# Optimization experiments

Hardware: AMD Instinct MI355X
Metric: run time of the kernel (lower is better)

Reference implementation:

```python
import jax, jax.numpy as jnp
import numpy as np


def setup_inputs() -> dict:
    key = jax.random.key(0)
    k1, k2, k3 = jax.random.split(key, 3)
    B, T, D, U = 64, 1024, 256, 256
    inputs = jax.random.normal(k1, (B, T, D), dtype=jnp.float32)
    W_xh = jax.random.normal(k2, (D, U), dtype=jnp.float32) * (1.0 / np.sqrt(D))
    W_hh = jax.random.normal(k3, (U, U), dtype=jnp.float32) * (1.0 / np.sqrt(U))
    b_h = jnp.zeros((U,), dtype=jnp.float32)
    return {"inputs": inputs, "W_xh": W_xh, "W_hh": W_hh, "b_h": b_h}


def reference(inputs, W_xh, W_hh, b_h):
    # inputs: [B, T, D]. Precompute input projection (same math as per-step matmul),
    # then scan the sequential recurrence: h_t = tanh(xW_t + h_{t-1} @ W_hh + b).
    B = inputs.shape[0]
    U = W_hh.shape[0]
    xW = jnp.einsum('btd,du->btu', inputs, W_xh) + b_h  # [B, T, U]
    h0 = jnp.zeros((B, U), dtype=inputs.dtype)

    def step(h, xw_t):
        h_new = jnp.tanh(xw_t + h @ W_hh)
        return h_new, h_new

    _, hs = jax.lax.scan(step, h0, jnp.swapaxes(xW, 0, 1))  # hs: [T, B, U]
    return jnp.swapaxes(hs, 0, 1)  # [B, T, U] (return_sequences=True)
```

## Files before the change

kernel.cpp:

```cpp
#include <hip/hip_runtime.h>
#include <math.h>

#define B_ 64
#define T_ 1024
#define D_ 256
#define U_ 256

typedef __fp16   hf2_t __attribute__((ext_vector_type(2)));
typedef _Float16 f16x8 __attribute__((ext_vector_type(8)));
typedef float    f32x4 __attribute__((ext_vector_type(4)));

__device__ __forceinline__ float fast_tanh2(float x) {
    float e = __expf(2.0f * x);
    return 1.0f - 2.0f * __builtin_amdgcn_rcpf(e + 1.0f);
}

#define CH_  16
#define NCH_ (T_ / CH_)
#define NT2_ 512

__global__ __launch_bounds__(NT2_) __attribute__((amdgpu_waves_per_eu(2, 2)))
void rnn_fused(const float* __restrict__ inputs,
               const float* __restrict__ W_xh,
               const float* __restrict__ W_hh,
               const float* __restrict__ b_h,
               float* __restrict__ out) {
    const int b    = (int)blockIdx.x;
    const int tid  = (int)threadIdx.x;
    const int w    = tid >> 6;
    const int lane = tid & 63;
    const int g    = lane >> 4;
    const int c    = lane & 15;
    const int n0   = w * 32;

    __shared__ float xwb[2][CH_][U_];
    __shared__ __align__(16) _Float16 hl[2][U_];
    __shared__ __align__(16) _Float16 Ax[CH_ * D_];

    f16x8 whh[8][2], wxh[8][2];
    #pragma unroll
    for (int kt = 0; kt < 8; ++kt) {
        #pragma unroll
        for (int nt = 0; nt < 2; ++nt) {
            f16x8 vh, vx;
            #pragma unroll
            for (int j = 0; j < 8; ++j) {
                const int row = kt * 32 + g * 8 + j;
                const int col = n0 + nt * 16 + c;
                vh[j] = (_Float16)W_hh[(size_t)row * U_ + col];
                vx[j] = (_Float16)W_xh[(size_t)row * U_ + col];
            }
            whh[kt][nt] = vh;
            wxh[kt][nt] = vx;
        }
    }
    const float bb0 = b_h[n0 + c];
    const float bb1 = b_h[n0 + 16 + c];

    if (tid < 128) ((float*)&hl[0][0])[tid] = 0.f;

    const float* ibase = inputs + (size_t)b * T_ * D_;
    float* gbase = out + (size_t)b * T_ * U_;

    const int srow = tid >> 5;
    const int sk8  = (tid & 31) * 8;
    char* const sdst = (char*)Ax + srow * 512 + ((sk8 * 2) ^ ((srow & 7) << 4));
    const int vbaseA = c * 512 + ((g * 16) ^ ((c & 7) << 4));

    const f32x4 zero4 = {0.f, 0.f, 0.f, 0.f};

#define PACK8(DST, F0, F1)                                                    \
    {                                                                         \
        union { hf2_t p[4]; f16x8 v; } u;                                     \
        u.p[0] = __builtin_amdgcn_cvt_pkrtz((F0).x, (F0).y);                  \
        u.p[1] = __builtin_amdgcn_cvt_pkrtz((F0).z, (F0).w);                  \
        u.p[2] = __builtin_amdgcn_cvt_pkrtz((F1).x, (F1).y);                  \
        u.p[3] = __builtin_amdgcn_cvt_pkrtz((F1).z, (F1).w);                  \
        *(f16x8*)(DST) = u.v;                                                 \
    }

#define MFMA16(A, BF, ACC) \
    ACC = __builtin_amdgcn_mfma_f32_16x16x32_f16((A), (BF), (ACC), 0, 0, 0)

#define BAR()                                                                 \
    asm volatile("s_waitcnt lgkmcnt(0)" ::: "memory");                        \
    __builtin_amdgcn_s_barrier();                                             \
    asm volatile("" ::: "memory");

#define PROJECT(PB)                                                           \
    {                                                                         \
        f16x8 a0_ = *(const f16x8*)((const char*)Ax + (vbaseA ^ 0));          \
        f32x4 q0 = zero4, q1 = zero4, q2 = zero4, q3 = zero4;                 \
        MFMA16(a0_, wxh[0][0], q0); MFMA16(a0_, wxh[0][1], q1);               \
        _Pragma("unroll") for (int kt = 1; kt < 4; ++kt) {                    \
            f16x8 a = *(const f16x8*)((const char*)Ax + (vbaseA ^ (kt * 64)));\
            MFMA16(a, wxh[kt][0], q0); MFMA16(a, wxh[kt][1], q1);             \
        }                                                                     \
        _Pragma("unroll") for (int kt = 4; kt < 8; ++kt) {                    \
            f16x8 a = *(const f16x8*)((const char*)Ax + (vbaseA ^ (kt * 64)));\
            MFMA16(a, wxh[kt][0], q2); MFMA16(a, wxh[kt][1], q3);             \
        }                                                                     \
        _Pragma("unroll") for (int r = 0; r < 4; ++r) {                       \
            xwb[PB][g * 4 + r][n0 + c]      = q0[r] + q2[r] + bb0;            \
            xwb[PB][g * 4 + r][n0 + 16 + c] = q1[r] + q3[r] + bb1;            \
        }                                                                     \
    }

    {
        float4 f0 = *(const float4*)&ibase[8 * tid];
        float4 f1 = *(const float4*)&ibase[8 * tid + 4];
        PACK8(sdst, f0, f1)
    }
    __syncthreads();
    PROJECT(0)
    float4 p0, p1;
    {
        const float* gs = ibase + (size_t)CH_ * D_;
        p0 = *(const float4*)&gs[8 * tid];
        p1 = *(const float4*)&gs[8 * tid + 4];
    }
    BAR()

    const char* hrd = (const char*)&hl[0][0] + g * 16;
    char*       hwr = (char*)&hl[0][0] + (n0 + c) * 2;

#define STEP(J)                                                               \
    {                                                                         \
        const int RD = ((J) & 1) * 512;                                       \
        const int WR = 512 - RD;                                              \
        const float* bcf = &xwb[cur][(J)][n0 + c];                            \
        const float xw0 = bcf[0];                                             \
        const float xw1 = bcf[16];                                            \
        __builtin_amdgcn_s_setprio(1);                                        \
        f16x8 af0 = *(const f16x8*)(hrd + RD);                                \
        f32x4 ca0 = zero4, ca1 = zero4, cb0 = zero4, cb1 = zero4;             \
        MFMA16(af0, whh[0][0], ca0); MFMA16(af0, whh[0][1], ca1);             \
        _Pragma("unroll") for (int kt = 1; kt < 4; ++kt) {                    \
            f16x8 a = *(const f16x8*)(hrd + RD + 64 * kt);                    \
            MFMA16(a, whh[kt][0], ca0); MFMA16(a, whh[kt][1], ca1);           \
        }                                                                     \
        _Pragma("unroll") for (int kt = 4; kt < 8; ++kt) {                    \
            f16x8 a = *(const f16x8*)(hrd + RD + 64 * kt);                    \
            MFMA16(a, whh[kt][0], cb0); MFMA16(a, whh[kt][1], cb1);           \
        }                                                                     \
        __builtin_amdgcn_s_setprio(0);                                        \
        const float h0 = fast_tanh2(ca0[0] + cb0[0] + xw0);                   \
        const float h1 = fast_tanh2(ca1[0] + cb1[0] + xw1);                   \
        if (g == 0) {                                                         \
            *(_Float16*)(hwr + WR)      = (_Float16)h0;                       \
            *(_Float16*)(hwr + WR + 32) = (_Float16)h1;                       \
            float* go = gbase + (size_t)(ch * CH_ + (J)) * U_ + n0 + c;       \
            go[0]  = h0;                                                      \
            go[16] = h1;                                                      \
        }                                                                     \
        BAR()                                                                 \
    }

    int cur = 0;
    for (int ch = 0; ch < NCH_; ++ch) {
        STEP(0)  STEP(1)  STEP(2)  STEP(3)
        STEP(4)  STEP(5)  STEP(6)  STEP(7)
        STEP(8)  STEP(9)  STEP(10) STEP(11)
        STEP(12) STEP(13) STEP(14) STEP(15)

        if (ch + 1 < NCH_) { PACK8(sdst, p0, p1) }
        BAR()
        if (ch + 1 < NCH_) PROJECT(1 - cur)
        if (ch + 2 < NCH_) {
            const float* gs = ibase + (size_t)(ch + 2) * CH_ * D_;
            p0 = *(const float4*)&gs[8 * tid];
            p1 = *(const float4*)&gs[8 * tid + 4];
        }
        BAR()
        cur ^= 1;
    }
#undef STEP
#undef PROJECT
#undef BAR
#undef MFMA16
#undef PACK8
}

extern "C" void kernel_launch(void* const* d_in, const int* in_sizes, int n_in,
                              void* d_out, int out_size, void* d_ws, size_t ws_size,
                              hipStream_t stream) {
    const float* inputs = (const float*)d_in[0];
    const float* W_xh   = (const float*)d_in[1];
    const float* W_hh   = (const float*)d_in[2];
    const float* b_h    = (const float*)d_in[3];
    float* out = (float*)d_out;

    rnn_fused<<<B_, NT2_, 0, stream>>>(inputs, W_xh, W_hh, b_h, out);
}
```

Measured before the change: 546.4 us.

## Keep input projection in registers and permute columns for packed stores

```diff
diff --git a/kernel.cpp b/kernel.cpp
--- a/kernel.cpp
+++ b/kernel.cpp
@@ -32,8 +32,8 @@
     const int g    = lane >> 4;
     const int c    = lane & 15;
     const int n0   = w * 32;
+    const int cp   = n0 + 2 * c;
 
-    __shared__ float xwb[2][CH_][U_];
     __shared__ __align__(16) _Float16 hl[2][U_];
     __shared__ __align__(16) _Float16 Ax[CH_ * D_];
 
@@ -46,16 +46,15 @@
             #pragma unroll
             for (int j = 0; j < 8; ++j) {
                 const int row = kt * 32 + g * 8 + j;
-                const int col = n0 + nt * 16 + c;
-                vh[j] = (_Float16)W_hh[(size_t)row * U_ + col];
-                vx[j] = (_Float16)W_xh[(size_t)row * U_ + col];
+                vh[j] = (_Float16)W_hh[(size_t)row * U_ + cp + nt];
+                vx[j] = (_Float16)W_xh[(size_t)row * U_ + cp + nt];
             }
             whh[kt][nt] = vh;
             wxh[kt][nt] = vx;
         }
     }
-    const float bb0 = b_h[n0 + c];
-    const float bb1 = b_h[n0 + 16 + c];
+    const float bb0 = b_h[cp];
+    const float bb1 = b_h[cp + 1];
 
     if (tid < 128) ((float*)&hl[0][0])[tid] = 0.f;
 
@@ -87,12 +86,12 @@
     __builtin_amdgcn_s_barrier();                                             \
     asm volatile("" ::: "memory");
 
-#define PROJECT(PB)                                                           \
+    f32x4 qa = zero4, qb = zero4;
+
+#define PROJECT()                                                             \
     {                                                                         \
-        f16x8 a0_ = *(const f16x8*)((const char*)Ax + (vbaseA ^ 0));          \
         f32x4 q0 = zero4, q1 = zero4, q2 = zero4, q3 = zero4;                 \
-        MFMA16(a0_, wxh[0][0], q0); MFMA16(a0_, wxh[0][1], q1);               \
-        _Pragma("unroll") for (int kt = 1; kt < 4; ++kt) {                    \
+        _Pragma("unroll") for (int kt = 0; kt < 4; ++kt) {                    \
             f16x8 a = *(const f16x8*)((const char*)Ax + (vbaseA ^ (kt * 64)));\
             MFMA16(a, wxh[kt][0], q0); MFMA16(a, wxh[kt][1], q1);             \
         }                                                                     \
@@ -101,8 +100,8 @@
             MFMA16(a, wxh[kt][0], q2); MFMA16(a, wxh[kt][1], q3);             \
         }                                                                     \
         _Pragma("unroll") for (int r = 0; r < 4; ++r) {                       \
-            xwb[PB][g * 4 + r][n0 + c]      = q0[r] + q2[r] + bb0;            \
-            xwb[PB][g * 4 + r][n0 + 16 + c] = q1[r] + q3[r] + bb1;            \
+            qa[r] = q0[r] + q2[r] + bb0;                                      \
+            qb[r] = q1[r] + q3[r] + bb1;                                      \
         }                                                                     \
     }
 
@@ -112,7 +111,7 @@
         PACK8(sdst, f0, f1)
     }
     __syncthreads();
-    PROJECT(0)
+    PROJECT()
     float4 p0, p1;
     {
         const float* gs = ibase + (size_t)CH_ * D_;
@@ -122,15 +121,12 @@
     BAR()
 
     const char* hrd = (const char*)&hl[0][0] + g * 16;
-    char*       hwr = (char*)&hl[0][0] + (n0 + c) * 2;
+    char*       hwr = (char*)&hl[0][0] + cp * 2;
 
 #define STEP(J)                                                               \
     {                                                                         \
         const int RD = ((J) & 1) * 512;                                       \
         const int WR = 512 - RD;                                              \
-        const float* bcf = &xwb[cur][(J)][n0 + c];                            \
-        const float xw0 = bcf[0];                                             \
-        const float xw1 = bcf[16];                                            \
         __builtin_amdgcn_s_setprio(1);                                        \
         f16x8 af0 = *(const f16x8*)(hrd + RD);                                \
         f32x4 ca0 = zero4, ca1 = zero4, cb0 = zero4, cb1 = zero4;             \
@@ -144,19 +140,16 @@
             MFMA16(a, whh[kt][0], cb0); MFMA16(a, whh[kt][1], cb1);           \
         }                                                                     \
         __builtin_amdgcn_s_setprio(0);                                        \
-        const float h0 = fast_tanh2(ca0[0] + cb0[0] + xw0);                   \
-        const float h1 = fast_tanh2(ca1[0] + cb1[0] + xw1);                   \
-        if (g == 0) {                                                         \
-            *(_Float16*)(hwr + WR)      = (_Float16)h0;                       \
-            *(_Float16*)(hwr + WR + 32) = (_Float16)h1;                       \
-            float* go = gbase + (size_t)(ch * CH_ + (J)) * U_ + n0 + c;       \
-            go[0]  = h0;                                                      \
-            go[16] = h1;                                                      \
+        if (g == ((J) >> 2)) {                                                \
+            const float h0 = fast_tanh2(ca0[0] + cb0[0] + qa[(J) & 3]);       \
+            const float h1 = fast_tanh2(ca1[0] + cb1[0] + qb[(J) & 3]);       \
+            *(hf2_t*)(hwr + WR) = __builtin_amdgcn_cvt_pkrtz(h0, h1);         \
+            float* go = gbase + (size_t)(ch * CH_ + (J)) * U_ + cp;           \
+            *(float2*)go = make_float2(h0, h1);                               \
         }                                                                     \
         BAR()                                                                 \
     }
 
-    int cur = 0;
     for (int ch = 0; ch < NCH_; ++ch) {
         STEP(0)  STEP(1)  STEP(2)  STEP(3)
         STEP(4)  STEP(5)  STEP(6)  STEP(7)
@@ -165,14 +158,12 @@
 
         if (ch + 1 < NCH_) { PACK8(sdst, p0, p1) }
         BAR()
-        if (ch + 1 < NCH_) PROJECT(1 - cur)
+        if (ch + 1 < NCH_) PROJECT()
         if (ch + 2 < NCH_) {
             const float* gs = ibase + (size_t)(ch + 2) * CH_ * D_;
             p0 = *(const float4*)&gs[8 * tid];
             p1 = *(const float4*)&gs[8 * tid + 4];
         }
-        BAR()
-        cur ^= 1;
     }
 #undef STEP
 #undef PROJECT
```

After: 516.8 us. -5.4%, faster.
